# Optimization experiments

Hardware: AMD Instinct MI355X
Metric: run time of the kernel (lower is better)

The kernel has to match this reference:

```python
import jax, jax.numpy as jnp
import numpy as np

B, A, C, H, S, NR = 128, 2048, 128, 512, 3, 2
PR = C + 3 + S   # 134 read params per head
PW = 3 * C + 3 + S  # 390 write params


def setup_inputs() -> dict:
    key = jax.random.key(0)
    ks = jax.random.split(key, 8)
    h = jax.random.normal(ks[0], (B, H), jnp.float32)
    mem = jax.random.normal(ks[1], (B, A, C), jnp.float32)
    ra = jax.random.uniform(ks[2], (NR, B, A), jnp.float32)
    ra = ra / ra.sum(-1, keepdims=True)  # valid attention distributions
    wa = jax.random.uniform(ks[3], (B, A), jnp.float32)
    wa = wa / wa.sum(-1, keepdims=True)
    W_read = 0.02 * jax.random.normal(ks[4], (NR, PR, H), jnp.float32)
    b_read = jnp.zeros((NR, PR), jnp.float32)
    W_write = 0.02 * jax.random.normal(ks[5], (PW, H), jnp.float32)
    b_write = jnp.zeros((PW,), jnp.float32)
    return dict(h=h, mem=mem, prev_read_attn=ra, prev_write_attn=wa,
                W_read=W_read, b_read=b_read, W_write=W_write, b_write=b_write)


def _addressing(query, beta, gate, shift, gamma, mem, prev_w):
    """NTM addressing. query [...,C] (raw), beta/gate/gamma [...,1], shift [...,S],
    mem [B,A,C] (broadcasts), prev_w [...,A]. Returns attention [...,A]."""
    eps = 1e-8
    q = jax.nn.sigmoid(query)
    beta = jax.nn.softplus(beta) + 1.0
    gate = jax.nn.sigmoid(gate)
    shift_w = jax.nn.softmax(shift, axis=-1)
    gamma = jax.nn.softplus(gamma) + 1.0
    # content-based addressing: cosine similarity + sharpened softmax over A
    qn = jnp.maximum(jnp.linalg.norm(q, axis=-1, keepdims=True), eps)      # [...,1]
    mn = jnp.maximum(jnp.linalg.norm(mem, axis=-1), eps)                   # [B,A]
    sim = jnp.einsum('...c,...ac->...a', q, mem) / (qn * mn)
    w_c = jax.nn.softmax(beta * sim, axis=-1)
    # gated interpolation with previous attention
    w_g = gate * w_c + (1.0 - gate) * prev_w
    # circular shift convolution, offsets -(S//2)..S//2
    K = S // 2
    idx = (jnp.arange(A)[:, None] - (jnp.arange(S)[None, :] - K)) % A      # [A,S]
    w_s = jnp.einsum('...as,...s->...a', w_g[..., idx], shift_w)
    # gamma sharpening
    w_pow = w_s ** gamma
    return w_pow / (w_pow.sum(-1, keepdims=True) + 1e-12)


def reference(h, mem, prev_read_attn, prev_write_attn, W_read, b_read, W_write, b_write):
    # --- read heads (vectorized over NR heads) ---
    pr = jnp.einsum('bh,rph->rbp', h, W_read) + b_read[:, None, :]         # [NR,B,PR]
    q, beta, gate, shift, gamma = jnp.split(pr, [C, C + 1, C + 2, C + 2 + S], axis=-1)
    read_w = _addressing(q, beta, gate, shift, gamma, mem, prev_read_attn)  # [NR,B,A]
    read_vectors = jnp.einsum('rba,bac->rbc', read_w, mem)                 # [NR,B,C]
    # --- write head ---
    pw = h @ W_write.T + b_write                                           # [B,PW]
    locs = np.cumsum([C, 1, 1, S, 1, C])
    qw, bw, gw, sw, gmw, erase, add = jnp.split(pw, locs.tolist(), axis=-1)
    write_w = _addressing(qw, bw, gw, sw, gmw, mem, prev_write_attn)       # [B,A]
    e = jax.nn.sigmoid(erase)[:, None, :]                                  # [B,1,C]
    a = jax.nn.sigmoid(add)[:, None, :]                                    # [B,1,C]
    w = write_w[..., None]                                                 # [B,A,1]
    new_mem = mem * (1.0 - w * e) + w * a
    return read_vectors, new_mem
```

## Files before the change

### kernel.cpp

```cpp
#include <hip/hip_runtime.h>
#include <math.h>

constexpr int B_  = 128;
constexpr int A_  = 2048;
constexpr int C_  = 128;
constexpr int H_  = 512;
constexpr int S_  = 3;
constexpr int NR_ = 2;
constexpr int PR_ = C_ + 3 + S_;
constexpr int PW_ = 3 * C_ + 3 + S_;

typedef float vfloat4 __attribute__((ext_vector_type(4)));

__device__ __forceinline__ float sigmoidf_(float x) { return 1.0f / (1.0f + expf(-x)); }
__device__ __forceinline__ float softplusf_(float x) {
  return fmaxf(x, 0.0f) + log1pf(expf(-fabsf(x)));
}

__device__ __forceinline__ float waveReduceSum(float v) {
#pragma unroll
  for (int off = 32; off; off >>= 1) v += __shfl_xor(v, off, 64);
  return v;
}
__device__ __forceinline__ float waveReduceMax(float v) {
#pragma unroll
  for (int off = 32; off; off >>= 1) v = fmaxf(v, __shfl_xor(v, off, 64));
  return v;
}

__device__ __forceinline__ float blockReduceSum(float v, float* rbuf) {
  int tid = threadIdx.x;
  v = waveReduceSum(v);
  if ((tid & 63) == 0) rbuf[tid >> 6] = v;
  __syncthreads();
  float r = rbuf[0] + rbuf[1] + rbuf[2] + rbuf[3];
  __syncthreads();
  return r;
}
__device__ __forceinline__ float blockReduceMax(float v, float* rbuf) {
  int tid = threadIdx.x;
  v = waveReduceMax(v);
  if ((tid & 63) == 0) rbuf[tid >> 6] = v;
  __syncthreads();
  float r = fmaxf(fmaxf(rbuf[0], rbuf[1]), fmaxf(rbuf[2], rbuf[3]));
  __syncthreads();
  return r;
}

__global__ __launch_bounds__(256) void proj_kernel(
    const float* __restrict__ h, const float* __restrict__ Wr,
    const float* __restrict__ br, const float* __restrict__ Ww,
    const float* __restrict__ bw, float* __restrict__ pr, float* __restrict__ pw) {
  constexpr int NPR = NR_ * B_ * PR_;
  constexpr int NPW = B_ * PW_;
  int wave = (blockIdx.x * blockDim.x + threadIdx.x) >> 6;
  int lane = threadIdx.x & 63;
  const float* wrow;
  const float* hrow;
  float bias;
  float* outp;
  if (wave < NPR) {
    int r = wave / (B_ * PR_);
    int rem = wave - r * (B_ * PR_);
    int b = rem / PR_;
    int p = rem - b * PR_;
    wrow = Wr + (size_t)(r * PR_ + p) * H_;
    hrow = h + (size_t)b * H_;
    bias = br[r * PR_ + p];
    outp = pr + wave;
  } else {
    int w2 = wave - NPR;
    if (w2 >= NPW) return;
    int b = w2 / PW_;
    int p = w2 - b * PW_;
    wrow = Ww + (size_t)p * H_;
    hrow = h + (size_t)b * H_;
    bias = bw[p];
    outp = pw + w2;
  }
  const float4* w4 = (const float4*)wrow;
  const float4* h4 = (const float4*)hrow;
  float4 a0 = h4[(lane << 1)];
  float4 a1 = h4[(lane << 1) + 1];
  float4 b0 = w4[(lane << 1)];
  float4 b1 = w4[(lane << 1) + 1];
  float acc = a0.x * b0.x;
  acc = fmaf(a0.y, b0.y, acc);
  acc = fmaf(a0.z, b0.z, acc);
  acc = fmaf(a0.w, b0.w, acc);
  acc = fmaf(a1.x, b1.x, acc);
  acc = fmaf(a1.y, b1.y, acc);
  acc = fmaf(a1.z, b1.z, acc);
  acc = fmaf(a1.w, b1.w, acc);
  acc = waveReduceSum(acc);
  if (lane == 0) *outp = acc + bias;
}

__global__ __launch_bounds__(64) void headprep_kernel(
    const float* __restrict__ pr, const float* __restrict__ pw,
    float* __restrict__ qbuf, float* __restrict__ qn, float* __restrict__ pars,
    float* __restrict__ rv) {
  int hb = blockIdx.x;
  int hd = hb >> 7;
  int b = hb & (B_ - 1);
  int lane = threadIdx.x;
  for (int i = hb * 64 + lane; i < NR_ * B_ * C_; i += 384 * 64) rv[i] = 0.0f;

  const float* src = (hd < 2) ? (pr + (size_t)hb * PR_) : (pw + (size_t)b * PW_);
  float2 raw = ((const float2*)src)[lane];
  float q0 = sigmoidf_(raw.x);
  float q1 = sigmoidf_(raw.y);
  ((float2*)(qbuf + (size_t)hb * C_))[lane] = make_float2(q0, q1);
  float ss = q0 * q0 + q1 * q1;
  ss = waveReduceSum(ss);
  if (lane == 0) {
    qn[hb] = fmaxf(sqrtf(ss), 1e-8f);
    float braw = src[C_];
    float graw = src[C_ + 1];
    float s0 = src[C_ + 2], s1 = src[C_ + 3], s2 = src[C_ + 4];
    float gmraw = src[C_ + 5];
    float mx = fmaxf(s0, fmaxf(s1, s2));
    float e0 = expf(s0 - mx), e1 = expf(s1 - mx), e2 = expf(s2 - mx);
    float inv = 1.0f / (e0 + e1 + e2);
    float* pp = pars + hb * 8;
    pp[0] = softplusf_(braw) + 1.0f;
    pp[1] = sigmoidf_(graw);
    pp[2] = e0 * inv;
    pp[3] = e1 * inv;
    pp[4] = e2 * inv;
    pp[5] = softplusf_(gmraw) + 1.0f;
  }
}

__global__ __launch_bounds__(256) void sim_kernel(
    const float* __restrict__ mem, const float* __restrict__ qbuf,
    const float* __restrict__ qn, float* __restrict__ sim) {
  __shared__ __align__(16) float qs[3 * C_];
  __shared__ float qnl[3];
  int b = blockIdx.x >> 5;
  int chunk = blockIdx.x & 31;
  int rowbase = chunk << 6;
  int tid = threadIdx.x;
  for (int idx = tid; idx < 3 * C_; idx += 256) {
    int hd = idx >> 7;
    int c = idx & (C_ - 1);
    qs[idx] = qbuf[(size_t)(hd * B_ + b) * C_ + c];
  }
  if (tid < 3) qnl[tid] = qn[tid * B_ + b];
  __syncthreads();

  int wv = tid >> 6;
  int lane = tid & 63;
  int j = lane & 7;
  int rsub = lane >> 3;

  float4 q0[4], q1[4], q2[4];
  const float4* qs4 = (const float4*)qs;
#pragma unroll
  for (int k = 0; k < 4; k++) {
    q0[k] = qs4[j + 8 * k];
    q1[k] = qs4[32 + j + 8 * k];
    q2[k] = qs4[64 + j + 8 * k];
  }
  float iqn0 = 1.0f / qnl[0], iqn1 = 1.0f / qnl[1], iqn2 = 1.0f / qnl[2];

#pragma unroll
  for (int it = 0; it < 2; it++) {
    int row = rowbase + (it << 5) + (wv << 3) + rsub;
    const float4* mrow = (const float4*)(mem + ((size_t)b * A_ + row) * C_);
    float d0 = 0.f, d1 = 0.f, d2 = 0.f, ss = 0.f;
#pragma unroll
    for (int k = 0; k < 4; k++) {
      float4 m = mrow[j + 8 * k];
      d0 = fmaf(m.x, q0[k].x, d0); d0 = fmaf(m.y, q0[k].y, d0);
      d0 = fmaf(m.z, q0[k].z, d0); d0 = fmaf(m.w, q0[k].w, d0);
      d1 = fmaf(m.x, q1[k].x, d1); d1 = fmaf(m.y, q1[k].y, d1);
      d1 = fmaf(m.z, q1[k].z, d1); d1 = fmaf(m.w, q1[k].w, d1);
      d2 = fmaf(m.x, q2[k].x, d2); d2 = fmaf(m.y, q2[k].y, d2);
      d2 = fmaf(m.z, q2[k].z, d2); d2 = fmaf(m.w, q2[k].w, d2);
      ss = fmaf(m.x, m.x, ss); ss = fmaf(m.y, m.y, ss);
      ss = fmaf(m.z, m.z, ss); ss = fmaf(m.w, m.w, ss);
    }
#pragma unroll
    for (int off = 1; off <= 4; off <<= 1) {
      d0 += __shfl_xor(d0, off, 64);
      d1 += __shfl_xor(d1, off, 64);
      d2 += __shfl_xor(d2, off, 64);
      ss += __shfl_xor(ss, off, 64);
    }
    if (j == 0) {
      float imn = 1.0f / fmaxf(sqrtf(ss), 1e-8f);
      sim[(size_t)(0 * B_ + b) * A_ + row] = d0 * iqn0 * imn;
      sim[(size_t)(1 * B_ + b) * A_ + row] = d1 * iqn1 * imn;
      sim[(size_t)(2 * B_ + b) * A_ + row] = d2 * iqn2 * imn;
    }
  }
}

__global__ __launch_bounds__(256) void attn_kernel(
    const float* __restrict__ sim, const float* __restrict__ ra,
    const float* __restrict__ wa, const float* __restrict__ pars,
    float* __restrict__ attn) {
  __shared__ float wg[A_];
  __shared__ float rbuf[4];
  int hb = blockIdx.x;
  int hd = hb >> 7;
  int b = hb & (B_ - 1);
  int tid = threadIdx.x;
  const float* pp = pars + hb * 8;
  float beta = pp[0], gate = pp[1], sw0 = pp[2], sw1 = pp[3], sw2 = pp[4], gamma = pp[5];
  const float* simrow = sim + (size_t)hb * A_;
  const float* prev = (hd < 2) ? (ra + (size_t)hb * A_) : (wa + (size_t)b * A_);
  float* outrow = attn + (size_t)hb * A_;

  float s[8];
  float mx = -1e30f;
#pragma unroll
  for (int i = 0; i < 8; i++) {
    s[i] = simrow[tid + (i << 8)];
    mx = fmaxf(mx, s[i]);
  }
  mx = blockReduceMax(mx, rbuf);
  float p[8];
  float lsum = 0.0f;
#pragma unroll
  for (int i = 0; i < 8; i++) {
    p[i] = expf(beta * (s[i] - mx));
    lsum += p[i];
  }
  float tot = blockReduceSum(lsum, rbuf);
  float inv = 1.0f / tot;
#pragma unroll
  for (int i = 0; i < 8; i++) {
    int a = tid + (i << 8);
    wg[a] = fmaf(gate, p[i] * inv, (1.0f - gate) * prev[a]);
  }
  __syncthreads();
  float lsum2 = 0.0f;
#pragma unroll
  for (int i = 0; i < 8; i++) {
    int a = tid + (i << 8);
    float ws = sw0 * wg[(a + 1) & (A_ - 1)] + sw1 * wg[a] + sw2 * wg[(a - 1) & (A_ - 1)];
    float wp = (ws > 0.0f) ? exp2f(gamma * log2f(ws)) : 0.0f;
    p[i] = wp;
    lsum2 += wp;
  }
  float tot2 = blockReduceSum(lsum2, rbuf);
  float inv2 = 1.0f / (tot2 + 1e-12f);
#pragma unroll
  for (int i = 0; i < 8; i++) {
    outrow[tid + (i << 8)] = p[i] * inv2;
  }
}

__global__ __launch_bounds__(256) void update_kernel(
    const float* __restrict__ mem, const float* __restrict__ attn,
    const float* __restrict__ pw, float* __restrict__ rv,
    float* __restrict__ nmem) {
  __shared__ float att0[256], att1[256], attw[256];
  __shared__ float4 red0[256];
  __shared__ float4 red1[256];
  int b = blockIdx.x >> 3;
  int chunk = blockIdx.x & 7;
  int rowbase = chunk << 8;
  int tid = threadIdx.x;
  att0[tid] = attn[(size_t)(0 * B_ + b) * A_ + rowbase + tid];
  att1[tid] = attn[(size_t)(1 * B_ + b) * A_ + rowbase + tid];
  attw[tid] = attn[(size_t)(2 * B_ + b) * A_ + rowbase + tid];
  __syncthreads();

  int rowlane = tid & 31;
  int rowoff = tid >> 5;
  int c0 = rowlane << 2;
  const float* pwrow = pw + (size_t)b * PW_;
  float2 eA = *(const float2*)(pwrow + C_ + 6 + c0);
  float2 eB = *(const float2*)(pwrow + C_ + 6 + c0 + 2);
  float2 aA = *(const float2*)(pwrow + 2 * C_ + 6 + c0);
  float2 aB = *(const float2*)(pwrow + 2 * C_ + 6 + c0 + 2);
  float e0 = sigmoidf_(eA.x), e1 = sigmoidf_(eA.y), e2 = sigmoidf_(eB.x), e3 = sigmoidf_(eB.y);
  float ad0 = sigmoidf_(aA.x), ad1 = sigmoidf_(aA.y), ad2 = sigmoidf_(aB.x), ad3 = sigmoidf_(aB.y);

  float4 acc0 = make_float4(0.f, 0.f, 0.f, 0.f);
  float4 acc1 = make_float4(0.f, 0.f, 0.f, 0.f);

#pragma unroll 4
  for (int i = 0; i < 32; i++) {
    int ridx = (i << 3) + rowoff;
    int row = rowbase + ridx;
    size_t base = ((size_t)b * A_ + row) * C_ + c0;
    float4 m = *(const float4*)(mem + base);
    float w0 = att0[ridx];
    float w1 = att1[ridx];
    float ww = attw[ridx];
    acc0.x = fmaf(w0, m.x, acc0.x);
    acc0.y = fmaf(w0, m.y, acc0.y);
    acc0.z = fmaf(w0, m.z, acc0.z);
    acc0.w = fmaf(w0, m.w, acc0.w);
    acc1.x = fmaf(w1, m.x, acc1.x);
    acc1.y = fmaf(w1, m.y, acc1.y);
    acc1.z = fmaf(w1, m.z, acc1.z);
    acc1.w = fmaf(w1, m.w, acc1.w);
    vfloat4 nm;
    nm.x = fmaf(m.x, 1.0f - ww * e0, ww * ad0);
    nm.y = fmaf(m.y, 1.0f - ww * e1, ww * ad1);
    nm.z = fmaf(m.z, 1.0f - ww * e2, ww * ad2);
    nm.w = fmaf(m.w, 1.0f - ww * e3, ww * ad3);
    __builtin_nontemporal_store(nm, (vfloat4*)(nmem + base));
  }

  red0[tid] = acc0;
  red1[tid] = acc1;
  __syncthreads();
#pragma unroll
  for (int s = 128; s >= 32; s >>= 1) {
    if (tid < s) {
      float4 x = red0[tid], y = red0[tid + s];
      x.x += y.x; x.y += y.y; x.z += y.z; x.w += y.w;
      red0[tid] = x;
      float4 u = red1[tid], v = red1[tid + s];
      u.x += v.x; u.y += v.y; u.z += v.z; u.w += v.w;
      red1[tid] = u;
    }
    __syncthreads();
  }
  if (tid < 32) {
    float4 r0 = red0[tid];
    float4 r1 = red1[tid];
    float* rv0 = rv + (size_t)(0 * B_ + b) * C_ + (tid << 2);
    float* rv1 = rv + (size_t)(1 * B_ + b) * C_ + (tid << 2);
    atomicAdd(rv0 + 0, r0.x);
    atomicAdd(rv0 + 1, r0.y);
    atomicAdd(rv0 + 2, r0.z);
    atomicAdd(rv0 + 3, r0.w);
    atomicAdd(rv1 + 0, r1.x);
    atomicAdd(rv1 + 1, r1.y);
    atomicAdd(rv1 + 2, r1.z);
    atomicAdd(rv1 + 3, r1.w);
  }
}

extern "C" void kernel_launch(void* const* d_in, const int* in_sizes, int n_in,
                              void* d_out, int out_size, void* d_ws, size_t ws_size,
                              hipStream_t stream) {
  const float* h   = (const float*)d_in[0];
  const float* mem = (const float*)d_in[1];
  const float* ra  = (const float*)d_in[2];
  const float* wa  = (const float*)d_in[3];
  const float* Wr  = (const float*)d_in[4];
  const float* br  = (const float*)d_in[5];
  const float* Ww  = (const float*)d_in[6];
  const float* bw  = (const float*)d_in[7];

  float* out = (float*)d_out;
  float* rv = out;
  float* nmem = out + NR_ * B_ * C_;

  float* ws = (float*)d_ws;
  float* pr_buf = ws;
  float* pw_buf = pr_buf + NR_ * B_ * PR_;
  float* qbuf   = pw_buf + B_ * PW_;
  float* qn     = qbuf + 3 * B_ * C_;
  float* pars   = qn + 3 * B_;
  float* simb   = pars + 3 * B_ * 8;

  constexpr int NWAVES = NR_ * B_ * PR_ + B_ * PW_;
  proj_kernel<<<dim3((NWAVES + 3) / 4), dim3(256), 0, stream>>>(h, Wr, br, Ww, bw, pr_buf, pw_buf);
  headprep_kernel<<<dim3(3 * B_), dim3(64), 0, stream>>>(pr_buf, pw_buf, qbuf, qn, pars, rv);
  sim_kernel<<<dim3(B_ * (A_ / 64)), dim3(256), 0, stream>>>(mem, qbuf, qn, simb);
  attn_kernel<<<dim3(3 * B_), dim3(256), 0, stream>>>(simb, ra, wa, pars, simb);
  update_kernel<<<dim3(B_ * (A_ / 256)), dim3(256), 0, stream>>>(mem, simb, pw_buf, rv, nmem);
}
```

Measured before the change: 291.8 us.

## Batch projection over 4 rows per block and fold headprep into sim/attn kernels

The projection kernel now stages four batch rows of h in shared memory, so each weight row read from global memory is reused across four batch entries instead of being reloaded per (batch, param) wave. The separate headprep launch is removed. Query sigmoid and norm are now computed inside sim_kernel, and the scalar head parameters are derived inside attn_kernel. This cuts one launch and the intermediate buffers, in exchange for redundant sigmoid/norm work repeated across the 32 sim blocks per batch.

Result: slower. 299.5 us (+2.7%).

```diff
diff --git a/kernel.cpp b/kernel.cpp
--- a/kernel.cpp
+++ b/kernel.cpp
@@ -9,6 +9,7 @@
 constexpr int NR_ = 2;
 constexpr int PR_ = C_ + 3 + S_;
 constexpr int PW_ = 3 * C_ + 3 + S_;
+constexpr int NOUT_ = NR_ * PR_ + PW_;
 
 typedef float vfloat4 __attribute__((ext_vector_type(4)));
 
@@ -50,103 +51,99 @@
 __global__ __launch_bounds__(256) void proj_kernel(
     const float* __restrict__ h, const float* __restrict__ Wr,
     const float* __restrict__ br, const float* __restrict__ Ww,
-    const float* __restrict__ bw, float* __restrict__ pr, float* __restrict__ pw) {
-  constexpr int NPR = NR_ * B_ * PR_;
-  constexpr int NPW = B_ * PW_;
-  int wave = (blockIdx.x * blockDim.x + threadIdx.x) >> 6;
-  int lane = threadIdx.x & 63;
-  const float* wrow;
-  const float* hrow;
-  float bias;
-  float* outp;
-  if (wave < NPR) {
-    int r = wave / (B_ * PR_);
-    int rem = wave - r * (B_ * PR_);
-    int b = rem / PR_;
-    int p = rem - b * PR_;
-    wrow = Wr + (size_t)(r * PR_ + p) * H_;
-    hrow = h + (size_t)b * H_;
-    bias = br[r * PR_ + p];
-    outp = pr + wave;
-  } else {
-    int w2 = wave - NPR;
-    if (w2 >= NPW) return;
-    int b = w2 / PW_;
-    int p = w2 - b * PW_;
-    wrow = Ww + (size_t)p * H_;
-    hrow = h + (size_t)b * H_;
-    bias = bw[p];
-    outp = pw + w2;
-  }
-  const float4* w4 = (const float4*)wrow;
-  const float4* h4 = (const float4*)hrow;
-  float4 a0 = h4[(lane << 1)];
-  float4 a1 = h4[(lane << 1) + 1];
-  float4 b0 = w4[(lane << 1)];
-  float4 b1 = w4[(lane << 1) + 1];
-  float acc = a0.x * b0.x;
-  acc = fmaf(a0.y, b0.y, acc);
-  acc = fmaf(a0.z, b0.z, acc);
-  acc = fmaf(a0.w, b0.w, acc);
-  acc = fmaf(a1.x, b1.x, acc);
-  acc = fmaf(a1.y, b1.y, acc);
-  acc = fmaf(a1.z, b1.z, acc);
-  acc = fmaf(a1.w, b1.w, acc);
-  acc = waveReduceSum(acc);
-  if (lane == 0) *outp = acc + bias;
-}
-
-__global__ __launch_bounds__(64) void headprep_kernel(
-    const float* __restrict__ pr, const float* __restrict__ pw,
-    float* __restrict__ qbuf, float* __restrict__ qn, float* __restrict__ pars,
-    float* __restrict__ rv) {
-  int hb = blockIdx.x;
-  int hd = hb >> 7;
-  int b = hb & (B_ - 1);
-  int lane = threadIdx.x;
-  for (int i = hb * 64 + lane; i < NR_ * B_ * C_; i += 384 * 64) rv[i] = 0.0f;
-
-  const float* src = (hd < 2) ? (pr + (size_t)hb * PR_) : (pw + (size_t)b * PW_);
-  float2 raw = ((const float2*)src)[lane];
-  float q0 = sigmoidf_(raw.x);
-  float q1 = sigmoidf_(raw.y);
-  ((float2*)(qbuf + (size_t)hb * C_))[lane] = make_float2(q0, q1);
-  float ss = q0 * q0 + q1 * q1;
-  ss = waveReduceSum(ss);
-  if (lane == 0) {
-    qn[hb] = fmaxf(sqrtf(ss), 1e-8f);
-    float braw = src[C_];
-    float graw = src[C_ + 1];
-    float s0 = src[C_ + 2], s1 = src[C_ + 3], s2 = src[C_ + 4];
-    float gmraw = src[C_ + 5];
-    float mx = fmaxf(s0, fmaxf(s1, s2));
-    float e0 = expf(s0 - mx), e1 = expf(s1 - mx), e2 = expf(s2 - mx);
-    float inv = 1.0f / (e0 + e1 + e2);
-    float* pp = pars + hb * 8;
-    pp[0] = softplusf_(braw) + 1.0f;
-    pp[1] = sigmoidf_(graw);
-    pp[2] = e0 * inv;
-    pp[3] = e1 * inv;
-    pp[4] = e2 * inv;
-    pp[5] = softplusf_(gmraw) + 1.0f;
+    const float* __restrict__ bw, float* __restrict__ pr,
+    float* __restrict__ pw, float* __restrict__ rv) {
+  __shared__ __align__(16) float4 hs4[4 * (H_ / 4)];
+  int bg = blockIdx.x >> 3;
+  int slice = blockIdx.x & 7;
+  int tid = threadIdx.x;
+
+  int gid = blockIdx.x * 256 + tid;
+  if (gid < NR_ * B_ * C_) rv[gid] = 0.0f;
+
+  const float4* h4g = (const float4*)h;
+  for (int i = tid; i < 512; i += 256) {
+    int bl = i >> 7;
+    int f = i & 127;
+    hs4[i] = h4g[((size_t)(bg * 4 + bl)) * (H_ / 4) + f];
+  }
+  __syncthreads();
+
+  int wv = tid >> 6;
+  int lane = tid & 63;
+  float4 hv[4][2];
+#pragma unroll
+  for (int bl = 0; bl < 4; bl++) {
+    hv[bl][0] = hs4[bl * 128 + lane];
+    hv[bl][1] = hs4[bl * 128 + 64 + lane];
+  }
+
+  for (int j = wv; j * 8 + slice < NOUT_; j += 4) {
+    int o = j * 8 + slice;
+    const float* wrow;
+    float bias;
+    if (o < NR_ * PR_) {
+      wrow = Wr + (size_t)o * H_;
+      bias = br[o];
+    } else {
+      wrow = Ww + (size_t)(o - NR_ * PR_) * H_;
+      bias = bw[o - NR_ * PR_];
+    }
+    const float4* w4 = (const float4*)wrow;
+    float4 w0 = w4[lane];
+    float4 w1 = w4[lane + 64];
+    float acc[4];
+#pragma unroll
+    for (int bl = 0; bl < 4; bl++) {
+      float a = hv[bl][0].x * w0.x;
+      a = fmaf(hv[bl][0].y, w0.y, a);
+      a = fmaf(hv[bl][0].z, w0.z, a);
+      a = fmaf(hv[bl][0].w, w0.w, a);
+      a = fmaf(hv[bl][1].x, w1.x, a);
+      a = fmaf(hv[bl][1].y, w1.y, a);
+      a = fmaf(hv[bl][1].z, w1.z, a);
+      a = fmaf(hv[bl][1].w, w1.w, a);
+      acc[bl] = waveReduceSum(a);
+    }
+    if (lane == 0) {
+#pragma unroll
+      for (int bl = 0; bl < 4; bl++) {
+        int b = bg * 4 + bl;
+        if (o < NR_ * PR_) {
+          int r = (o >= PR_) ? 1 : 0;
+          int p = o - r * PR_;
+          pr[((size_t)(r * B_ + b)) * PR_ + p] = acc[bl] + bias;
+        } else {
+          pw[(size_t)b * PW_ + (o - NR_ * PR_)] = acc[bl] + bias;
+        }
+      }
+    }
   }
 }
 
 __global__ __launch_bounds__(256) void sim_kernel(
-    const float* __restrict__ mem, const float* __restrict__ qbuf,
-    const float* __restrict__ qn, float* __restrict__ sim) {
+    const float* __restrict__ mem, const float* __restrict__ pr,
+    const float* __restrict__ pw, float* __restrict__ sim) {
   __shared__ __align__(16) float qs[3 * C_];
   __shared__ float qnl[3];
   int b = blockIdx.x >> 5;
   int chunk = blockIdx.x & 31;
   int rowbase = chunk << 6;
   int tid = threadIdx.x;
-  for (int idx = tid; idx < 3 * C_; idx += 256) {
-    int hd = idx >> 7;
-    int c = idx & (C_ - 1);
-    qs[idx] = qbuf[(size_t)(hd * B_ + b) * C_ + c];
-  }
-  if (tid < 3) qnl[tid] = qn[tid * B_ + b];
+
+  if (tid < 192) {
+    int hd = tid >> 6;
+    int c2 = (tid & 63) << 1;
+    const float* src = (hd < 2) ? (pr + ((size_t)(hd * B_ + b)) * PR_)
+                                : (pw + (size_t)b * PW_);
+    float2 raw = *(const float2*)(src + c2);
+    float q0 = sigmoidf_(raw.x);
+    float q1 = sigmoidf_(raw.y);
+    qs[hd * C_ + c2] = q0;
+    qs[hd * C_ + c2 + 1] = q1;
+    float ss = waveReduceSum(q0 * q0 + q1 * q1);
+    if ((tid & 63) == 0) qnl[hd] = fmaxf(sqrtf(ss), 1e-8f);
+  }
   __syncthreads();
 
   int wv = tid >> 6;
@@ -199,16 +196,31 @@
 
 __global__ __launch_bounds__(256) void attn_kernel(
     const float* __restrict__ sim, const float* __restrict__ ra,
-    const float* __restrict__ wa, const float* __restrict__ pars,
-    float* __restrict__ attn) {
+    const float* __restrict__ wa, const float* __restrict__ pr,
+    const float* __restrict__ pw, float* __restrict__ attn) {
   __shared__ float wg[A_];
   __shared__ float rbuf[4];
+  __shared__ float pp[6];
   int hb = blockIdx.x;
   int hd = hb >> 7;
   int b = hb & (B_ - 1);
   int tid = threadIdx.x;
-  const float* pp = pars + hb * 8;
-  float beta = pp[0], gate = pp[1], sw0 = pp[2], sw1 = pp[3], sw2 = pp[4], gamma = pp[5];
+  const float* src = (hd < 2) ? (pr + (size_t)hb * PR_) : (pw + (size_t)b * PW_);
+  if (tid == 0) {
+    float braw = src[C_];
+    float graw = src[C_ + 1];
+    float s0 = src[C_ + 2], s1 = src[C_ + 3], s2 = src[C_ + 4];
+    float gmraw = src[C_ + 5];
+    float mx3 = fmaxf(s0, fmaxf(s1, s2));
+    float e0 = expf(s0 - mx3), e1 = expf(s1 - mx3), e2 = expf(s2 - mx3);
+    float inv3 = 1.0f / (e0 + e1 + e2);
+    pp[0] = softplusf_(braw) + 1.0f;
+    pp[1] = sigmoidf_(graw);
+    pp[2] = e0 * inv3;
+    pp[3] = e1 * inv3;
+    pp[4] = e2 * inv3;
+    pp[5] = softplusf_(gmraw) + 1.0f;
+  }
   const float* simrow = sim + (size_t)hb * A_;
   const float* prev = (hd < 2) ? (ra + (size_t)hb * A_) : (wa + (size_t)b * A_);
   float* outrow = attn + (size_t)hb * A_;
@@ -221,6 +233,7 @@
     mx = fmaxf(mx, s[i]);
   }
   mx = blockReduceMax(mx, rbuf);
+  float beta = pp[0], gate = pp[1], sw0 = pp[2], sw1 = pp[3], sw2 = pp[4], gamma = pp[5];
   float p[8];
   float lsum = 0.0f;
 #pragma unroll
@@ -358,15 +371,10 @@
   float* ws = (float*)d_ws;
   float* pr_buf = ws;
   float* pw_buf = pr_buf + NR_ * B_ * PR_;
-  float* qbuf   = pw_buf + B_ * PW_;
-  float* qn     = qbuf + 3 * B_ * C_;
-  float* pars   = qn + 3 * B_;
-  float* simb   = pars + 3 * B_ * 8;
-
-  constexpr int NWAVES = NR_ * B_ * PR_ + B_ * PW_;
-  proj_kernel<<<dim3((NWAVES + 3) / 4), dim3(256), 0, stream>>>(h, Wr, br, Ww, bw, pr_buf, pw_buf);
-  headprep_kernel<<<dim3(3 * B_), dim3(64), 0, stream>>>(pr_buf, pw_buf, qbuf, qn, pars, rv);
-  sim_kernel<<<dim3(B_ * (A_ / 64)), dim3(256), 0, stream>>>(mem, qbuf, qn, simb);
-  attn_kernel<<<dim3(3 * B_), dim3(256), 0, stream>>>(simb, ra, wa, pars, simb);
+  float* simb   = pw_buf + B_ * PW_;
+
+  proj_kernel<<<dim3(256), dim3(256), 0, stream>>>(h, Wr, br, Ww, bw, pr_buf, pw_buf, rv);
+  sim_kernel<<<dim3(B_ * (A_ / 64)), dim3(256), 0, stream>>>(mem, pr_buf, pw_buf, simb);
+  attn_kernel<<<dim3(3 * B_), dim3(256), 0, stream>>>(simb, ra, wa, pr_buf, pw_buf, simb);
   update_kernel<<<dim3(B_ * (A_ / 256)), dim3(256), 0, stream>>>(mem, simb, pw_buf, rv, nmem);
 }
```
